# Kernel optimization log

Measured on AMD Instinct MI355X. Metric: run time of the kernel, lower is better.

## Reference

```python
import jax, jax.numpy as jnp
import numpy as np

N_EMBD = 768
N_HEAD = 12
EPS = 1e-5

def setup_inputs() -> dict:
    key = jax.random.key(0)
    ks = jax.random.split(key, 13)
    C = N_EMBD
    s = lambda n: 1.0 / np.sqrt(n)
    return {
        "x":      jax.random.normal(ks[0], (2, 2048, C), dtype=jnp.float32),
        "ln1_w":  jnp.ones((C,), jnp.float32),
        "ln1_b":  jnp.zeros((C,), jnp.float32),
        "w_qkv":  jax.random.normal(ks[1], (C, 3 * C), dtype=jnp.float32) * s(C),
        "b_qkv":  jnp.zeros((3 * C,), jnp.float32),
        "w_proj": jax.random.normal(ks[2], (C, C), dtype=jnp.float32) * s(C),
        "b_proj": jnp.zeros((C,), jnp.float32),
        "ln2_w":  jnp.ones((C,), jnp.float32),
        "ln2_b":  jnp.zeros((C,), jnp.float32),
        "w_fc1":  jax.random.normal(ks[3], (C, 4 * C), dtype=jnp.float32) * s(C),
        "b_fc1":  jnp.zeros((4 * C,), jnp.float32),
        "w_fc2":  jax.random.normal(ks[4], (4 * C, C), dtype=jnp.float32) * s(4 * C),
        "b_fc2":  jnp.zeros((C,), jnp.float32),
    }

def _layernorm(x, w, b):
    mu = jnp.mean(x, axis=-1, keepdims=True)
    var = jnp.mean(jnp.square(x - mu), axis=-1, keepdims=True)
    return (x - mu) * jax.lax.rsqrt(var + EPS) * w + b

def reference(x, ln1_w, ln1_b, w_qkv, b_qkv, w_proj, b_proj,
              ln2_w, ln2_b, w_fc1, b_fc1, w_fc2, b_fc2):
    B, T, C = x.shape
    H = N_HEAD
    hd = C // H
    # --- attention branch ---
    h = _layernorm(x, ln1_w, ln1_b)
    qkv = h @ w_qkv + b_qkv                                  # [B,T,3C]
    q, k, v = jnp.split(qkv, 3, axis=-1)
    q = q.reshape(B, T, H, hd).transpose(0, 2, 1, 3)          # [B,H,T,hd]
    k = k.reshape(B, T, H, hd).transpose(0, 2, 1, 3)
    v = v.reshape(B, T, H, hd).transpose(0, 2, 1, 3)
    att = jnp.einsum('bhqd,bhkd->bhqk', q, k) * (1.0 / np.sqrt(hd))
    causal = jnp.tril(jnp.ones((T, T), dtype=bool))
    att = jnp.where(causal, att, -jnp.inf)
    att = jax.nn.softmax(att, axis=-1)
    y = jnp.einsum('bhqk,bhkd->bhqd', att, v)                 # [B,H,T,hd]
    y = y.transpose(0, 2, 1, 3).reshape(B, T, C)
    x = x + (y @ w_proj + b_proj)
    # --- MLP branch (dropout = identity in eval) ---
    h = _layernorm(x, ln2_w, ln2_b)
    h = jax.nn.gelu(h @ w_fc1 + b_fc1, approximate=False)
    x = x + (h @ w_fc2 + b_fc2)
    return x
```

## Files before the change

### kernel.cpp

```cpp
#include <hip/hip_runtime.h>
#include <math.h>

typedef __attribute__((ext_vector_type(8))) short short8;
typedef __attribute__((ext_vector_type(4))) float floatx4;

__device__ __forceinline__ unsigned short f2bf(float f) {
    union { float f; unsigned u; } v; v.f = f;
    unsigned r = v.u + 0x7fffu + ((v.u >> 16) & 1u);
    return (unsigned short)(r >> 16);
}

__device__ __forceinline__ float bf2f(unsigned short h) {
    union { unsigned u; float f; } v; v.u = ((unsigned)h) << 16; return v.f;
}

__device__ __forceinline__ float fexp2(float x) {
#if __has_builtin(__builtin_amdgcn_exp2f)
    return __builtin_amdgcn_exp2f(x);
#else
    return __expf(x * 0.69314718056f);
#endif
}

__device__ __forceinline__ void gload16(const unsigned short* g, unsigned short* l) {
    __builtin_amdgcn_global_load_lds(
        (const __attribute__((address_space(1))) unsigned int*)g,
        (__attribute__((address_space(3))) unsigned int*)l, 16, 0, 0);
}

__global__ __launch_bounds__(256) void ln_kernel(const float* __restrict__ x,
                                                 const float* __restrict__ w,
                                                 const float* __restrict__ b,
                                                 unsigned short* __restrict__ o) {
    int row = blockIdx.x, tid = threadIdx.x;
    const float* xr = x + (size_t)row * 768;
    float v0 = xr[tid], v1 = xr[tid + 256], v2 = xr[tid + 512];
    float s = v0 + v1 + v2, ss = v0 * v0 + v1 * v1 + v2 * v2;
#pragma unroll
    for (int o_ = 32; o_; o_ >>= 1) { s += __shfl_xor(s, o_); ss += __shfl_xor(ss, o_); }
    __shared__ float red[8];
    if ((tid & 63) == 0) { red[tid >> 6] = s; red[(tid >> 6) + 4] = ss; }
    __syncthreads();
    s = red[0] + red[1] + red[2] + red[3];
    ss = red[4] + red[5] + red[6] + red[7];
    float mu = s * (1.f / 768.f);
    float var = ss * (1.f / 768.f) - mu * mu;
    float inv = rsqrtf(var + 1e-5f);
    unsigned short* orow = o + (size_t)row * 768;
    orow[tid]       = f2bf((v0 - mu) * inv * w[tid]       + b[tid]);
    orow[tid + 256] = f2bf((v1 - mu) * inv * w[tid + 256] + b[tid + 256]);
    orow[tid + 512] = f2bf((v2 - mu) * inv * w[tid + 512] + b[tid + 512]);
}

__global__ __launch_bounds__(256) void wt_kernel(const float* __restrict__ w,
                                                 unsigned short* __restrict__ wt,
                                                 int K, int N) {
    __shared__ float t[32][33];
    int n0 = blockIdx.x * 32, k0 = blockIdx.y * 32;
    int tx = threadIdx.x & 31, ty = threadIdx.x >> 5;
#pragma unroll
    for (int i = 0; i < 32; i += 8)
        t[ty + i][tx] = w[(size_t)(k0 + ty + i) * N + n0 + tx];
    __syncthreads();
#pragma unroll
    for (int i = 0; i < 32; i += 8)
        wt[(size_t)(n0 + ty + i) * K + k0 + tx] = f2bf(t[tx][ty + i]);
}

template <int EPI>
__global__ __launch_bounds__(256) void gemm_kernel(
    const unsigned short* __restrict__ A, const unsigned short* __restrict__ Bt,
    const float* __restrict__ bias, const float* __restrict__ resid,
    float* __restrict__ fout, unsigned short* __restrict__ o0,
    unsigned short* __restrict__ o1, unsigned short* __restrict__ o2, int K) {
    __shared__ unsigned short Al[2][128 * 32];
    __shared__ unsigned short Bl[2][128 * 32];
    int tid = threadIdx.x, lane = tid & 63, w = tid >> 6;
    int wm = w >> 1, wn = w & 1;
    int nwg = (int)(gridDim.x * gridDim.y);
    int wgid = (int)(blockIdx.y * gridDim.x + blockIdx.x);
    int logical = (wgid & 7) * (nwg >> 3) + (wgid >> 3);
    int by = logical & 31, bx = logical >> 5;
    int m0 = by * 128, n0 = bx * 128;
    int lr = lane & 15, lk = (lane >> 4) << 3;

    int srow = w * 32 + (lane >> 2);
    int sko = (lane & 3) << 3;
    const unsigned short* Ab = A + (size_t)(m0 + srow) * K + sko;
    const unsigned short* Bb = Bt + (size_t)(n0 + srow) * K + sko;

    floatx4 acc[4][4];
#pragma unroll
    for (int i = 0; i < 4; i++)
#pragma unroll
        for (int j = 0; j < 4; j++) acc[i][j] = (floatx4){0.f, 0.f, 0.f, 0.f};

    int nk = K >> 5;
    auto stage = [&](int buf, int t) {
        int k0 = t << 5;
        unsigned short* Alp = &Al[buf][(w * 32) * 32];
        unsigned short* Blp = &Bl[buf][(w * 32) * 32];
        gload16(Ab + k0, Alp);
        gload16(Ab + 16 * K + k0, Alp + 16 * 32);
        gload16(Bb + k0, Blp);
        gload16(Bb + 16 * K + k0, Blp + 16 * 32);
    };

    stage(0, 0);
    for (int t = 0; t < nk; t++) {
        int cur = t & 1;
        __syncthreads();
        if (t + 1 < nk) stage(cur ^ 1, t + 1);
        short8 af[4], bfr[4];
#pragma unroll
        for (int mt = 0; mt < 4; mt++) af[mt] = *(short8*)&Al[cur][(wm * 64 + mt * 16 + lr) * 32 + lk];
#pragma unroll
        for (int nt = 0; nt < 4; nt++) bfr[nt] = *(short8*)&Bl[cur][(wn * 64 + nt * 16 + lr) * 32 + lk];
#pragma unroll
        for (int mt = 0; mt < 4; mt++)
#pragma unroll
            for (int nt = 0; nt < 4; nt++)
                acc[mt][nt] = __builtin_amdgcn_mfma_f32_16x16x32_bf16(af[mt], bfr[nt], acc[mt][nt], 0, 0, 0);
    }

    int mb = m0 + wm * 64, nb = n0 + wn * 64;
    int sec = 0;
    if (EPI == 0) sec = n0 / 768;
#pragma unroll
    for (int mt = 0; mt < 4; mt++)
#pragma unroll
        for (int nt = 0; nt < 4; nt++)
#pragma unroll
            for (int r = 0; r < 4; r++) {
                int mrow = mb + mt * 16 + ((lane >> 4) << 2) + r;
                int ncol = nb + nt * 16 + lr;
                float val = acc[mt][nt][r] + bias[ncol];
                if (EPI == 0) {
                    int f = ncol - sec * 768;
                    int h = f >> 6, d = f & 63;
                    int bb = mrow >> 11, t = mrow & 2047;
                    if (sec == 0)
                        o0[((size_t)(bb * 12 + h) * 2048 + t) * 64 + d] = f2bf(val * 0.1803368801f);
                    else if (sec == 1)
                        o1[((size_t)(bb * 12 + h) * 2048 + t) * 64 + d] = f2bf(val);
                    else
                        o2[((size_t)(bb * 12 + h) * 64 + d) * 2048 + t] = f2bf(val);
                } else if (EPI == 1) {
                    fout[(size_t)mrow * 768 + ncol] = val + resid[(size_t)mrow * 768 + ncol];
                } else if (EPI == 2) {
                    float g = 0.5f * val * (1.f + erff(val * 0.70710678118f));
                    o0[(size_t)mrow * 3072 + ncol] = f2bf(g);
                } else {
                    fout[(size_t)mrow * 768 + ncol] = val + resid[(size_t)mrow * 768 + ncol];
                }
            }
}

__global__ __launch_bounds__(256) void attn_kernel(const unsigned short* __restrict__ q_s,
                                                   const unsigned short* __restrict__ k_s,
                                                   const unsigned short* __restrict__ v_t,
                                                   unsigned short* __restrict__ y,
                                                   unsigned short* __restrict__ opart,
                                                   float* __restrict__ lpart) {
    __shared__ unsigned short KVs[2][8192];
    __shared__ unsigned short Pls[4][32][72];
    const int T = 2048, H = 12;
    int tid = threadIdx.x, lane = tid & 63, w = tid >> 6;
    int xx = (int)blockIdx.x;
    int bq, c;
    if (xx < 16)      { c = 0; bq = xx; }
    else if (xx < 28) { c = 1; bq = xx - 12; }
    else if (xx < 36) { c = 2; bq = xx - 20; }
    else              { c = 3; bq = xx - 24; }
    int bh = blockIdx.y;
    int bi = bh / H, hh = bh - bi * H;
    const unsigned short* qp = q_s + (size_t)bh * T * 64;
    const unsigned short* kp = k_s + (size_t)bh * T * 64;
    const unsigned short* vp = v_t + (size_t)bh * 64 * T;
    int wq0 = bq * 128 + w * 32;
    int lr = lane & 15, lk8 = (lane >> 4) << 3, hi = lane >> 4;
    int nt_blk = 2 * bq + 2;
    int t0 = c * 8;
    int t1 = t0 + 8 < nt_blk ? t0 + 8 : nt_blk;

    unsigned short (*Pl)[72] = Pls[w];

    int srow = tid >> 3, ssl = tid & 7;

    auto stage = [&](int buf, int t) {
        int kv0 = t * 64;
        unsigned short* base = &KVs[buf][(tid >> 6) * 512];
#pragma unroll
        for (int h = 0; h < 2; h++) {
            int r = srow + h * 32;
            int ss = ssl ^ (r & 7);
            gload16(kp + (size_t)(kv0 + r) * 64 + ss * 8, base + h * 2048);
            gload16(vp + (size_t)r * T + kv0 + ss * 8, base + 4096 + h * 2048);
        }
    };

    short8 aq[2][2];
#pragma unroll
    for (int mt = 0; mt < 2; mt++)
#pragma unroll
        for (int kf = 0; kf < 2; kf++)
            aq[mt][kf] = *(const short8*)&qp[(size_t)(wq0 + mt * 16 + lr) * 64 + kf * 32 + lk8];

    floatx4 yacc[2][4];
    float lacc[2][4];
#pragma unroll
    for (int i = 0; i < 2; i++)
#pragma unroll
        for (int j = 0; j < 4; j++) {
            yacc[i][j] = (floatx4){0.f, 0.f, 0.f, 0.f};
            lacc[i][j] = 0.f;
        }

    stage(0, t0);
    __syncthreads();

    for (int t = t0; t < t1; t++) {
        int cur = (t - t0) & 1;
        if (t + 1 < t1) stage(cur ^ 1, t + 1);
        int kv0 = t * 64;
        if (kv0 <= wq0 + 31) {
            const unsigned short* Kt = &KVs[cur][0];
            const unsigned short* Vt = &KVs[cur][4096];
            floatx4 sacc[2][4];
#pragma unroll
            for (int i = 0; i < 2; i++)
#pragma unroll
                for (int j = 0; j < 4; j++) sacc[i][j] = (floatx4){0.f, 0.f, 0.f, 0.f};
#pragma unroll
            for (int kf = 0; kf < 2; kf++) {
                int sl = ((kf << 2) | hi) ^ (lr & 7);
                short8 bk[4];
#pragma unroll
                for (int nt = 0; nt < 4; nt++)
                    bk[nt] = *(const short8*)&Kt[(nt * 16 + lr) * 64 + sl * 8];
#pragma unroll
                for (int mt = 0; mt < 2; mt++)
#pragma unroll
                    for (int nt = 0; nt < 4; nt++)
                        sacc[mt][nt] = __builtin_amdgcn_mfma_f32_16x16x32_bf16(aq[mt][kf], bk[nt], sacc[mt][nt], 0, 0, 0);
            }
            bool full = (kv0 + 63 <= wq0);
#pragma unroll
            for (int mt = 0; mt < 2; mt++)
#pragma unroll
                for (int r = 0; r < 4; r++) {
                    int qg = wq0 + mt * 16 + (hi << 2) + r;
                    int prow = mt * 16 + (hi << 2) + r;
#pragma unroll
                    for (int nt = 0; nt < 4; nt++) {
                        float sv = sacc[mt][nt][r];
                        if (!full) {
                            int kvg = kv0 + nt * 16 + lr;
                            sv = (kvg <= qg) ? sv : -1e30f;
                        }
                        float p = fexp2(sv);
                        lacc[mt][r] += p;
                        Pl[prow][nt * 16 + lr] = f2bf(p);
                    }
                }
#pragma unroll
            for (int kf = 0; kf < 2; kf++) {
                int sl = ((kf << 2) | hi) ^ (lr & 7);
                short8 pa[2], bv[4];
#pragma unroll
                for (int mt = 0; mt < 2; mt++) pa[mt] = *(short8*)&Pl[mt * 16 + lr][kf * 32 + lk8];
#pragma unroll
                for (int nt = 0; nt < 4; nt++)
                    bv[nt] = *(const short8*)&Vt[(nt * 16 + lr) * 64 + sl * 8];
#pragma unroll
                for (int mt = 0; mt < 2; mt++)
#pragma unroll
                    for (int nt = 0; nt < 4; nt++)
                        yacc[mt][nt] = __builtin_amdgcn_mfma_f32_16x16x32_bf16(pa[mt], bv[nt], yacc[mt][nt], 0, 0, 0);
            }
        }
        __syncthreads();
    }

    if (bq < 4) {
#pragma unroll
        for (int mt = 0; mt < 2; mt++)
#pragma unroll
            for (int r = 0; r < 4; r++) {
                float l = lacc[mt][r];
                l += __shfl_xor(l, 1);
                l += __shfl_xor(l, 2);
                l += __shfl_xor(l, 4);
                l += __shfl_xor(l, 8);
                float inv = 1.f / l;
                int qg = wq0 + mt * 16 + (hi << 2) + r;
#pragma unroll
                for (int nt = 0; nt < 4; nt++)
                    y[((size_t)(bi * T + qg)) * 768 + hh * 64 + nt * 16 + lr] = f2bf(yacc[mt][nt][r] * inv);
            }
    } else {
        int g = bq >> 2, rr = bq & 3;
        int base = (g == 1) ? 2 * rr : (g == 2) ? 8 + 3 * rr : 20 + 4 * rr;
        int slab = bh * 36 + base + c;
        unsigned short* op = opart + (size_t)slab * 8192;
        float* lp = lpart + (size_t)slab * 128;
#pragma unroll
        for (int mt = 0; mt < 2; mt++)
#pragma unroll
            for (int r = 0; r < 4; r++) {
                float l = lacc[mt][r];
                l += __shfl_xor(l, 1);
                l += __shfl_xor(l, 2);
                l += __shfl_xor(l, 4);
                l += __shfl_xor(l, 8);
                int wrow = w * 32 + mt * 16 + (hi << 2) + r;
                if (lr == 0) lp[wrow] = l;
#pragma unroll
                for (int nt = 0; nt < 4; nt++)
                    op[(size_t)wrow * 64 + nt * 16 + lr] = f2bf(yacc[mt][nt][r]);
            }
    }
}

__global__ __launch_bounds__(256) void attn_combine(const unsigned short* __restrict__ opart,
                                                    const float* __restrict__ lpart,
                                                    unsigned short* __restrict__ y) {
    const int T = 2048, H = 12;
    int bq = 4 + (int)blockIdx.x;
    int bh = blockIdx.y;
    int bi = bh / H, hh = bh - bi * H;
    int nchunk = (bq >> 2) + 1;
    int g = bq >> 2, rr = bq & 3;
    int base = (g == 1) ? 2 * rr : (g == 2) ? 8 + 3 * rr : 20 + 4 * rr;
    int tid = threadIdx.x;
    int row = tid >> 1, cb = (tid & 1) * 32;

    float l = 0.f;
    for (int c = 0; c < nchunk; c++) l += lpart[(size_t)(bh * 36 + base + c) * 128 + row];
    float inv = 1.f / l;

    float s[32];
#pragma unroll
    for (int j = 0; j < 32; j++) s[j] = 0.f;
    for (int c = 0; c < nchunk; c++) {
        const unsigned short* op = opart + ((size_t)(bh * 36 + base + c) * 128 + row) * 64 + cb;
#pragma unroll
        for (int v = 0; v < 4; v++) {
            short8 ob = *(const short8*)&op[v * 8];
#pragma unroll
            for (int j = 0; j < 8; j++) s[v * 8 + j] += bf2f((unsigned short)ob[j]);
        }
    }
    int qg = bq * 128 + row;
    unsigned short* yr = y + ((size_t)(bi * T + qg)) * 768 + hh * 64 + cb;
#pragma unroll
    for (int v = 0; v < 4; v++) {
        short8 ob;
#pragma unroll
        for (int j = 0; j < 8; j++) ob[j] = (short)f2bf(s[v * 8 + j] * inv);
        *(short8*)&yr[v * 8] = ob;
    }
}

extern "C" void kernel_launch(void* const* d_in, const int* in_sizes, int n_in,
                              void* d_out, int out_size, void* d_ws, size_t ws_size,
                              hipStream_t stream) {
    const float* x    = (const float*)d_in[0];
    const float* ln1w = (const float*)d_in[1];
    const float* ln1b = (const float*)d_in[2];
    const float* wqkv = (const float*)d_in[3];
    const float* bqkv = (const float*)d_in[4];
    const float* wproj= (const float*)d_in[5];
    const float* bproj= (const float*)d_in[6];
    const float* ln2w = (const float*)d_in[7];
    const float* ln2b = (const float*)d_in[8];
    const float* wfc1 = (const float*)d_in[9];
    const float* bfc1 = (const float*)d_in[10];
    const float* wfc2 = (const float*)d_in[11];
    const float* bfc2 = (const float*)d_in[12];
    float* out = (float*)d_out;

    char* ws = (char*)d_ws;
    size_t off = 0;
    auto alloc = [&](size_t bytes) { void* p = ws + off; off += (bytes + 255) & ~(size_t)255; return p; };

    const size_t MT = 4096;
    unsigned short* wqkv_t = (unsigned short*)alloc(2304 * 768 * 2);
    unsigned short* wproj_t= (unsigned short*)alloc(768 * 768 * 2);
    unsigned short* wfc1_t = (unsigned short*)alloc(3072 * 768 * 2);
    unsigned short* wfc2_t = (unsigned short*)alloc(768 * 3072 * 2);
    unsigned short* h12    = (unsigned short*)alloc(MT * 768 * 2);
    float*          x1     = (float*)alloc(MT * 768 * 4);
    unsigned short* qs     = (unsigned short*)alloc(MT * 768 * 2);
    unsigned short* ks     = (unsigned short*)alloc(MT * 768 * 2);
    unsigned short* vt     = (unsigned short*)alloc(MT * 768 * 2);
    unsigned short* yb     = (unsigned short*)alloc(MT * 768 * 2);
    unsigned short* hm     = qs;
    unsigned short* opart  = (unsigned short*)alloc(24 * 36 * 8192 * 2);
    float*          lpart  = (float*)alloc(24 * 36 * 128 * 4);

    wt_kernel<<<dim3(2304 / 32, 768 / 32), 256, 0, stream>>>(wqkv, wqkv_t, 768, 2304);
    wt_kernel<<<dim3(768 / 32, 768 / 32), 256, 0, stream>>>(wproj, wproj_t, 768, 768);
    wt_kernel<<<dim3(3072 / 32, 768 / 32), 256, 0, stream>>>(wfc1, wfc1_t, 768, 3072);
    wt_kernel<<<dim3(768 / 32, 3072 / 32), 256, 0, stream>>>(wfc2, wfc2_t, 3072, 768);

    ln_kernel<<<4096, 256, 0, stream>>>(x, ln1w, ln1b, h12);
    gemm_kernel<0><<<dim3(18, 32), 256, 0, stream>>>(h12, wqkv_t, bqkv, nullptr, nullptr, qs, ks, vt, 768);
    attn_kernel<<<dim3(40, 24), 256, 0, stream>>>(qs, ks, vt, yb, opart, lpart);
    attn_combine<<<dim3(12, 24), 256, 0, stream>>>(opart, lpart, yb);
    gemm_kernel<1><<<dim3(6, 32), 256, 0, stream>>>(yb, wproj_t, bproj, x, x1, nullptr, nullptr, nullptr, 768);
    ln_kernel<<<4096, 256, 0, stream>>>(x1, ln2w, ln2b, h12);
    gemm_kernel<2><<<dim3(24, 32), 256, 0, stream>>>(h12, wfc1_t, bfc1, nullptr, nullptr, hm, nullptr, nullptr, 768);
    gemm_kernel<3><<<dim3(6, 32), 256, 0, stream>>>(hm, wfc2_t, bfc2, x1, out, nullptr, nullptr, nullptr, 3072);
}
```

Baseline: 240.5 us.

## Split-K the fc2 GEMM into four chunks with a bf16 partial-sum combine kernel

The fc2 GEMM (K=3072) previously launched only 192 workgroups, each looping over the full K. It now launches 768 workgroups that each handle a 768-wide K chunk and write bf16 partials into reused workspace buffers. A new combine kernel then sums the four partials and adds the bias and residual. This should fill more of the device's compute units and shorten each block's serial K loop. In exchange it adds an extra kernel launch and partial-sum memory traffic, and rounding partials to bf16 costs some accuracy.

New measurement: 215.8 us. 1.11x faster.

```diff
diff --git a/kernel.cpp b/kernel.cpp
--- a/kernel.cpp
+++ b/kernel.cpp
@@ -72,7 +72,8 @@
     const unsigned short* __restrict__ A, const unsigned short* __restrict__ Bt,
     const float* __restrict__ bias, const float* __restrict__ resid,
     float* __restrict__ fout, unsigned short* __restrict__ o0,
-    unsigned short* __restrict__ o1, unsigned short* __restrict__ o2, int K) {
+    unsigned short* __restrict__ o1, unsigned short* __restrict__ o2,
+    int K, int Kcnt) {
     __shared__ unsigned short Al[2][128 * 32];
     __shared__ unsigned short Bl[2][128 * 32];
     int tid = threadIdx.x, lane = tid & 63, w = tid >> 6;
@@ -81,13 +82,21 @@
     int wgid = (int)(blockIdx.y * gridDim.x + blockIdx.x);
     int logical = (wgid & 7) * (nwg >> 3) + (wgid >> 3);
     int by = logical & 31, bx = logical >> 5;
-    int m0 = by * 128, n0 = bx * 128;
+    int m0 = by * 128;
+    int n0, kof = 0, chunk = 0;
+    if (EPI == 4) {
+        n0 = (bx % 6) * 128;
+        chunk = bx / 6;
+        kof = chunk * 768;
+    } else {
+        n0 = bx * 128;
+    }
     int lr = lane & 15, lk = (lane >> 4) << 3;
 
     int srow = w * 32 + (lane >> 2);
     int sko = (lane & 3) << 3;
-    const unsigned short* Ab = A + (size_t)(m0 + srow) * K + sko;
-    const unsigned short* Bb = Bt + (size_t)(n0 + srow) * K + sko;
+    const unsigned short* Ab = A + (size_t)(m0 + srow) * K + kof + sko;
+    const unsigned short* Bb = Bt + (size_t)(n0 + srow) * K + kof + sko;
 
     floatx4 acc[4][4];
 #pragma unroll
@@ -95,7 +104,7 @@
 #pragma unroll
         for (int j = 0; j < 4; j++) acc[i][j] = (floatx4){0.f, 0.f, 0.f, 0.f};
 
-    int nk = K >> 5;
+    int nk = Kcnt >> 5;
     auto stage = [&](int buf, int t) {
         int k0 = t << 5;
         unsigned short* Alp = &Al[buf][(w * 32) * 32];
@@ -134,7 +143,8 @@
             for (int r = 0; r < 4; r++) {
                 int mrow = mb + mt * 16 + ((lane >> 4) << 2) + r;
                 int ncol = nb + nt * 16 + lr;
-                float val = acc[mt][nt][r] + bias[ncol];
+                float val = acc[mt][nt][r];
+                if (EPI != 4) val += bias[ncol];
                 if (EPI == 0) {
                     int f = ncol - sec * 768;
                     int h = f >> 6, d = f & 63;
@@ -150,10 +160,34 @@
                 } else if (EPI == 2) {
                     float g = 0.5f * val * (1.f + erff(val * 0.70710678118f));
                     o0[(size_t)mrow * 3072 + ncol] = f2bf(g);
+                } else if (EPI == 3) {
+                    fout[(size_t)mrow * 768 + ncol] = val + resid[(size_t)mrow * 768 + ncol];
                 } else {
-                    fout[(size_t)mrow * 768 + ncol] = val + resid[(size_t)mrow * 768 + ncol];
+                    unsigned short* op = (chunk == 0) ? o0 : (chunk == 1) ? o1
+                                       : (chunk == 2) ? o2 : (unsigned short*)fout;
+                    op[(size_t)mrow * 768 + ncol] = f2bf(val);
                 }
             }
+}
+
+__global__ __launch_bounds__(256) void fc2_combine(
+    const unsigned short* __restrict__ p0, const unsigned short* __restrict__ p1,
+    const unsigned short* __restrict__ p2, const unsigned short* __restrict__ p3,
+    const float* __restrict__ bias, const float* __restrict__ resid,
+    float* __restrict__ out) {
+    int i = blockIdx.x * 256 + threadIdx.x;
+    size_t base = (size_t)i * 8;
+    int col = (int)(base % 768);
+    short8 a0 = *(const short8*)&p0[base];
+    short8 a1 = *(const short8*)&p1[base];
+    short8 a2 = *(const short8*)&p2[base];
+    short8 a3 = *(const short8*)&p3[base];
+#pragma unroll
+    for (int j = 0; j < 8; j++) {
+        float s = bf2f((unsigned short)a0[j]) + bf2f((unsigned short)a1[j]) +
+                  bf2f((unsigned short)a2[j]) + bf2f((unsigned short)a3[j]);
+        out[base + j] = s + bias[col + j] + resid[base + j];
+    }
 }
 
 __global__ __launch_bounds__(256) void attn_kernel(const unsigned short* __restrict__ q_s,
@@ -399,17 +433,23 @@
     unsigned short* opart  = (unsigned short*)alloc(24 * 36 * 8192 * 2);
     float*          lpart  = (float*)alloc(24 * 36 * 128 * 4);
 
+    unsigned short* p0 = (unsigned short*)ws;
+    unsigned short* p1 = opart;
+    unsigned short* p2 = (unsigned short*)((char*)opart + (size_t)MT * 768 * 2);
+    unsigned short* p3 = h12;
+
     wt_kernel<<<dim3(2304 / 32, 768 / 32), 256, 0, stream>>>(wqkv, wqkv_t, 768, 2304);
     wt_kernel<<<dim3(768 / 32, 768 / 32), 256, 0, stream>>>(wproj, wproj_t, 768, 768);
     wt_kernel<<<dim3(3072 / 32, 768 / 32), 256, 0, stream>>>(wfc1, wfc1_t, 768, 3072);
     wt_kernel<<<dim3(768 / 32, 3072 / 32), 256, 0, stream>>>(wfc2, wfc2_t, 3072, 768);
 
     ln_kernel<<<4096, 256, 0, stream>>>(x, ln1w, ln1b, h12);
-    gemm_kernel<0><<<dim3(18, 32), 256, 0, stream>>>(h12, wqkv_t, bqkv, nullptr, nullptr, qs, ks, vt, 768);
+    gemm_kernel<0><<<dim3(18, 32), 256, 0, stream>>>(h12, wqkv_t, bqkv, nullptr, nullptr, qs, ks, vt, 768, 768);
     attn_kernel<<<dim3(40, 24), 256, 0, stream>>>(qs, ks, vt, yb, opart, lpart);
     attn_combine<<<dim3(12, 24), 256, 0, stream>>>(opart, lpart, yb);
-    gemm_kernel<1><<<dim3(6, 32), 256, 0, stream>>>(yb, wproj_t, bproj, x, x1, nullptr, nullptr, nullptr, 768);
+    gemm_kernel<1><<<dim3(6, 32), 256, 0, stream>>>(yb, wproj_t, bproj, x, x1, nullptr, nullptr, nullptr, 768, 768);
     ln_kernel<<<4096, 256, 0, stream>>>(x1, ln2w, ln2b, h12);
-    gemm_kernel<2><<<dim3(24, 32), 256, 0, stream>>>(h12, wfc1_t, bfc1, nullptr, nullptr, hm, nullptr, nullptr, 768);
-    gemm_kernel<3><<<dim3(6, 32), 256, 0, stream>>>(hm, wfc2_t, bfc2, x1, out, nullptr, nullptr, nullptr, 3072);
-}
+    gemm_kernel<2><<<dim3(24, 32), 256, 0, stream>>>(h12, wfc1_t, bfc1, nullptr, nullptr, hm, nullptr, nullptr, 768, 768);
+    gemm_kernel<4><<<dim3(24, 32), 256, 0, stream>>>(hm, wfc2_t, nullptr, nullptr, (float*)p3, p0, p1, p2, 3072, 768);
+    fc2_combine<<<dim3(1536), 256, 0, stream>>>(p0, p1, p2, p3, bfc2, x1, out);
+}
```
